# Kernel optimization log

Hardware: AMD Instinct MI355X
Metric: run time of the kernel (lower is better)

## Reference

```python
import jax, jax.numpy as jnp
import numpy as np

N_TOKENS = 8192
TOP_K = 2
N_EXPERTS = 8
D_IN = 2048
D_OUT = 2048


def setup_inputs() -> dict:
    key = jax.random.key(0)
    k1, k2, k3, k4 = jax.random.split(key, 4)
    inputs = jax.random.normal(k1, (N_TOKENS, D_IN), dtype=jnp.float32)
    # stored as [E, out, in], matching nn.Parameter(torch.empty(E, output_size, input_size))
    expert_weights = 0.02 * jax.random.normal(k2, (N_EXPERTS, D_OUT, D_IN), dtype=jnp.float32)
    gates = jax.nn.softmax(jax.random.normal(k3, (N_TOKENS, TOP_K), dtype=jnp.float32), axis=-1)
    # per (token, slot) expert assignment, then sort by expert as the router would
    flat_experts = jax.random.randint(k4, (N_TOKENS * TOP_K,), 0, N_EXPERTS, dtype=jnp.int32)
    sorted_scattered_idxs = jnp.argsort(flat_experts).astype(jnp.int32)
    sorted_expert_idxs = flat_experts[sorted_scattered_idxs]
    expert_offsets = jnp.cumsum(jnp.bincount(flat_experts, length=N_EXPERTS)).astype(jnp.int32)
    return {
        "inputs": inputs,
        "expert_weights": expert_weights,
        "gates": gates,
        "k": TOP_K,
        "sorted_expert_idxs": sorted_expert_idxs,
        "sorted_scattered_idxs": sorted_scattered_idxs,
        "expert_offsets": expert_offsets,
    }


def reference(inputs, expert_weights, gates, k, sorted_expert_idxs, sorted_scattered_idxs, expert_offsets):
    N, d_in = inputs.shape
    E = expert_weights.shape[0]
    Nk = N * k
    # forward permutes weight [E, out, in] -> [E, in, out]
    W = jnp.transpose(expert_weights, (0, 2, 1))
    d_out = W.shape[-1]
    # invert the sort: expert id for each flat (token, slot) index
    expert_per_flat = jnp.zeros((Nk,), dtype=sorted_expert_idxs.dtype).at[
        sorted_scattered_idxs].set(sorted_expert_idxs)
    # scatter2scatter: out_flat[j] = x[j // k] @ W[expert_per_flat[j]]
    x_rep = jnp.repeat(inputs, k, axis=0)  # [N*k, d_in]
    out_flat = jnp.zeros((Nk, d_out), dtype=inputs.dtype)
    for e in range(E):  # small fixed expert count; masked grouped GEMM
        mask = (expert_per_flat == e)[:, None]
        out_flat = out_flat + jnp.where(mask, x_rep, 0.0) @ W[e]
    # combine: (gates.unsqueeze(1) @ output_expanded).squeeze(1)
    out = jnp.einsum('nk,nkd->nd', gates, out_flat.reshape(N, k, d_out))
    return out
```

## Files before the change

kernel.cpp:

```cpp
#include <hip/hip_runtime.h>
#include <hip/hip_bf16.h>
#include <stdint.h>

#define NTOK   8192
#define TOPK   2
#define NEXP   8
#define DIN    2048
#define DOUT   2048
#define NK     (NTOK*TOPK)

typedef __bf16 bf16_8 __attribute__((ext_vector_type(8)));
typedef float  f32x4  __attribute__((ext_vector_type(4)));

__device__ __forceinline__ void gl2lds16(const void* g, void* l) {
  auto gp = reinterpret_cast<const __attribute__((address_space(1))) uint32_t*>(
      reinterpret_cast<uintptr_t>(g));
  auto lp = reinterpret_cast<__attribute__((address_space(3))) uint32_t*>(
      reinterpret_cast<uintptr_t>(l));
  __builtin_amdgcn_global_load_lds(gp, lp, 16, 0, 0);
}

__global__ void cvt_f32_bf16(const float4* __restrict__ src,
                             uint4* __restrict__ dst, int n8) {
  int i = blockIdx.x * 256 + threadIdx.x;
  if (i >= n8) return;
  float4 a = src[2 * i];
  float4 b = src[2 * i + 1];
  union { __bf16 h[8]; uint4 u; } r;
  r.h[0] = (__bf16)a.x; r.h[1] = (__bf16)a.y; r.h[2] = (__bf16)a.z; r.h[3] = (__bf16)a.w;
  r.h[4] = (__bf16)b.x; r.h[5] = (__bf16)b.y; r.h[6] = (__bf16)b.z; r.h[7] = (__bf16)b.w;
  dst[i] = r.u;
}

__global__ __launch_bounds__(256)
void moe_gemm(const __bf16* __restrict__ X,
              const __bf16* __restrict__ W,
              const float* __restrict__ gates,
              const int* __restrict__ ssi,
              const int* __restrict__ offs,
              float* __restrict__ out)
{
  __shared__ __bf16 lA[128 * 32];
  __shared__ __bf16 lB[128 * 32];
  __shared__ int   sTok[128];
  __shared__ int   sDst[128];
  __shared__ float sGate[128];

  const int tid = threadIdx.x;
  const int bid = blockIdx.x;
  const int nt  = bid & 15;
  const int mtg = bid >> 4;

  int start = 0, end = 0, e, cum = 0, prev = 0, mloc = 0, found = 0;
  for (e = 0; e < NEXP; ++e) {
    int oe  = offs[e];
    int seg = oe - prev;
    int t   = (seg + 127) >> 7;
    if (mtg < cum + t) { start = prev; end = oe; mloc = mtg - cum; found = 1; break; }
    cum += t; prev = oe;
  }
  if (!found) return;

  const int m0 = start + mloc * 128;

  if (tid < 128) {
    int p     = m0 + tid;
    int valid = p < end;
    int f     = ssi[valid ? p : (end - 1)];
    int tok   = f >> 1;
    sTok[tid]  = tok;
    sDst[tid]  = valid ? tok : -1;
    sGate[tid] = valid ? gates[f] : 0.0f;
  }
  __syncthreads();

  const int rs = tid >> 2;
  const int kc = tid & 3;
  const __bf16* pA0 = X + (size_t)sTok[rs]      * DIN + kc * 8;
  const __bf16* pA1 = X + (size_t)sTok[rs + 64] * DIN + kc * 8;
  const __bf16* wB  = W + (size_t)e * DOUT * DIN + (size_t)(nt * 128) * DIN;
  const __bf16* pB0 = wB + (size_t)rs        * DIN + kc * 8;
  const __bf16* pB1 = wB + (size_t)(rs + 64) * DIN + kc * 8;
  char* ldsAb = (char*)lA + (tid & 192) * 16;
  char* ldsBb = (char*)lB + (tid & 192) * 16;

  const int w  = tid >> 6;
  const int l  = tid & 63;
  const int wm = w >> 1, wn = w & 1;
  const int lr = l & 15;
  const int kq = l >> 4;
  const __bf16* aBase = lA + (wm * 64 + lr) * 32 + kq * 8;
  const __bf16* bBase = lB + (wn * 64 + lr) * 32 + kq * 8;

  f32x4 acc[4][4] = {};

  for (int it = 0; it < DIN / 32; ++it) {
    __syncthreads();
    gl2lds16(pA0, ldsAb);
    gl2lds16(pA1, ldsAb + 4096);
    gl2lds16(pB0, ldsBb);
    gl2lds16(pB1, ldsBb + 4096);
    pA0 += 32; pA1 += 32; pB0 += 32; pB1 += 32;
    __syncthreads();

    bf16_8 af[4], bf[4];
#pragma unroll
    for (int am = 0; am < 4; ++am) af[am] = *(const bf16_8*)(aBase + am * 512);
#pragma unroll
    for (int bn = 0; bn < 4; ++bn) bf[bn] = *(const bf16_8*)(bBase + bn * 512);
#pragma unroll
    for (int am = 0; am < 4; ++am)
#pragma unroll
      for (int bn = 0; bn < 4; ++bn)
        acc[am][bn] = __builtin_amdgcn_mfma_f32_16x16x32_bf16(
            af[am], bf[bn], acc[am][bn], 0, 0, 0);
  }

  const int colBase = nt * 128 + wn * 64 + lr;
  const int rq = kq * 4;
#pragma unroll
  for (int am = 0; am < 4; ++am) {
#pragma unroll
    for (int v = 0; v < 4; ++v) {
      int rl = wm * 64 + am * 16 + rq + v;
      int t  = sDst[rl];
      if (t < 0) continue;
      float g = sGate[rl];
      float* orow = out + (size_t)t * DOUT + colBase;
#pragma unroll
      for (int bn = 0; bn < 4; ++bn)
        atomicAdd(orow + bn * 16, g * acc[am][bn][v]);
    }
  }
}

extern "C" void kernel_launch(void* const* d_in, const int* in_sizes, int n_in,
                              void* d_out, int out_size, void* d_ws, size_t ws_size,
                              hipStream_t stream) {
  const float* inputs = (const float*)d_in[0];
  const float* ew     = (const float*)d_in[1];
  const float* gates  = (const float*)d_in[2];
  const int*   ssi    = (const int*)d_in[5];
  const int*   offs   = (const int*)d_in[6];
  float* out = (float*)d_out;

  __bf16* wsW = (__bf16*)d_ws;
  __bf16* wsX = wsW + (size_t)NEXP * DOUT * DIN;

  const int n8w = NEXP * DOUT * DIN / 8;
  const int n8x = NTOK * DIN / 8;
  cvt_f32_bf16<<<n8w / 256, 256, 0, stream>>>((const float4*)ew, (uint4*)wsW, n8w);
  cvt_f32_bf16<<<n8x / 256, 256, 0, stream>>>((const float4*)inputs, (uint4*)wsX, n8x);
  hipMemsetAsync(d_out, 0, (size_t)NTOK * DOUT * sizeof(float), stream);

  moe_gemm<<<136 * 16, 256, 0, stream>>>(wsX, wsW, gates, ssi, offs, out);
}
```

Measured before the change: 510.8 us.

## Replace atomic scatter-add with bf16 flat output plus separate combine kernel

The GEMM no longer applies gates or atomically adds fp32 results into the token output. It writes each (token, slot) row as bf16 into a flat workspace, and a new combine kernel then does the gated sum of the two slots per token. This removes the output memset and the fp32 atomic traffic, at the cost of an extra launch, a round trip through the workspace, and bf16 rounding of the intermediate results. Launch bounds also request 4 blocks per CU.

```diff
diff --git a/kernel.cpp b/kernel.cpp
--- a/kernel.cpp
+++ b/kernel.cpp
@@ -32,19 +32,17 @@
   dst[i] = r.u;
 }
 
-__global__ __launch_bounds__(256)
+__global__ __launch_bounds__(256, 4)
 void moe_gemm(const __bf16* __restrict__ X,
               const __bf16* __restrict__ W,
-              const float* __restrict__ gates,
               const int* __restrict__ ssi,
               const int* __restrict__ offs,
-              float* __restrict__ out)
+              __bf16* __restrict__ flat)
 {
   __shared__ __bf16 lA[128 * 32];
   __shared__ __bf16 lB[128 * 32];
   __shared__ int   sTok[128];
-  __shared__ int   sDst[128];
-  __shared__ float sGate[128];
+  __shared__ int   sF[128];
 
   const int tid = threadIdx.x;
   const int bid = blockIdx.x;
@@ -67,10 +65,8 @@
     int p     = m0 + tid;
     int valid = p < end;
     int f     = ssi[valid ? p : (end - 1)];
-    int tok   = f >> 1;
-    sTok[tid]  = tok;
-    sDst[tid]  = valid ? tok : -1;
-    sGate[tid] = valid ? gates[f] : 0.0f;
+    sTok[tid] = f >> 1;
+    sF[tid]   = valid ? f : -1;
   }
   __syncthreads();
 
@@ -123,15 +119,32 @@
 #pragma unroll
     for (int v = 0; v < 4; ++v) {
       int rl = wm * 64 + am * 16 + rq + v;
-      int t  = sDst[rl];
-      if (t < 0) continue;
-      float g = sGate[rl];
-      float* orow = out + (size_t)t * DOUT + colBase;
+      int f  = sF[rl];
+      if (f < 0) continue;
+      __bf16* row = flat + (size_t)f * DOUT + colBase;
 #pragma unroll
       for (int bn = 0; bn < 4; ++bn)
-        atomicAdd(orow + bn * 16, g * acc[am][bn][v]);
+        row[bn * 16] = (__bf16)acc[am][bn][v];
     }
   }
+}
+
+__global__ __launch_bounds__(256)
+void combine(const __bf16* __restrict__ flat, const float* __restrict__ gates,
+             float* __restrict__ out) {
+  const int n = blockIdx.x;
+  const int c = threadIdx.x * 8;
+  bf16_8 y0 = *(const bf16_8*)(flat + (size_t)(2 * n)     * DOUT + c);
+  bf16_8 y1 = *(const bf16_8*)(flat + (size_t)(2 * n + 1) * DOUT + c);
+  const float g0 = gates[2 * n];
+  const float g1 = gates[2 * n + 1];
+  float o[8];
+#pragma unroll
+  for (int j = 0; j < 8; ++j)
+    o[j] = g0 * (float)y0[j] + g1 * (float)y1[j];
+  float4* dst = (float4*)(out + (size_t)n * DOUT + c);
+  dst[0] = *(float4*)&o[0];
+  dst[1] = *(float4*)&o[4];
 }
 
 extern "C" void kernel_launch(void* const* d_in, const int* in_sizes, int n_in,
@@ -146,12 +159,13 @@
 
   __bf16* wsW = (__bf16*)d_ws;
   __bf16* wsX = wsW + (size_t)NEXP * DOUT * DIN;
+  __bf16* wsF = wsX + (size_t)NTOK * DIN;
 
   const int n8w = NEXP * DOUT * DIN / 8;
   const int n8x = NTOK * DIN / 8;
   cvt_f32_bf16<<<n8w / 256, 256, 0, stream>>>((const float4*)ew, (uint4*)wsW, n8w);
   cvt_f32_bf16<<<n8x / 256, 256, 0, stream>>>((const float4*)inputs, (uint4*)wsX, n8x);
-  hipMemsetAsync(d_out, 0, (size_t)NTOK * DOUT * sizeof(float), stream);
 
-  moe_gemm<<<136 * 16, 256, 0, stream>>>(wsX, wsW, gates, ssi, offs, out);
+  moe_gemm<<<136 * 16, 256, 0, stream>>>(wsX, wsW, ssi, offs, wsF);
+  combine<<<NTOK, 256, 0, stream>>>(wsF, gates, out);
 }
```

Result: faster. 462.4 us (-9.5%).
